# Kernel optimization log

Hardware: AMD Instinct MI355X
Metric: run time of the kernel (lower is better)

The kernel has to match this reference:

```python
import jax, jax.numpy as jnp
import numpy as np

B, S, D, H, DEPTH, VOCAB = 4096, 64, 512, 8, 4, 2
HD = D // H
EPS = 1e-5


def setup_inputs() -> dict:
    key = jax.random.key(0)
    ks = jax.random.split(key, 12)
    sc = 0.02
    return {
        "a_seq": jax.random.randint(ks[0], (B, S), 0, VOCAB, dtype=jnp.int32),
        "b_seq": jax.random.randint(ks[1], (B, S), 0, VOCAB, dtype=jnp.int32),
        "bit_emb": jax.random.normal(ks[2], (VOCAB, D), jnp.float32),
        "start_state": jax.random.normal(ks[3], (D,), jnp.float32),
        "ln1_g": jnp.ones((DEPTH, D), jnp.float32),
        "ln1_b": jnp.zeros((DEPTH, D), jnp.float32),
        # weights stored [in, out] (transpose of torch nn.Linear layout)
        "qkv_w": jax.random.normal(ks[4], (DEPTH, D, 3 * D), jnp.float32) * sc,
        "qkv_b": jnp.zeros((DEPTH, 3 * D), jnp.float32),
        "out_w": jax.random.normal(ks[5], (DEPTH, D, D), jnp.float32) * sc,
        "out_b": jnp.zeros((DEPTH, D), jnp.float32),
        "ln2_g": jnp.ones((DEPTH, D), jnp.float32),
        "ln2_b": jnp.zeros((DEPTH, D), jnp.float32),
        "ff1_w": jax.random.normal(ks[6], (DEPTH, D, 4 * D), jnp.float32) * sc,
        "ff1_b": jnp.zeros((DEPTH, 4 * D), jnp.float32),
        "ff2_w": jax.random.normal(ks[7], (DEPTH, 4 * D, D), jnp.float32) * sc,
        "ff2_b": jnp.zeros((DEPTH, D), jnp.float32),
        "head_w": jax.random.normal(ks[8], (D, 2), jnp.float32) * sc,
        "head_b": jnp.zeros((2,), jnp.float32),
    }


def _ln(x, g, b):
    m = x.mean(-1, keepdims=True)
    c = x - m
    v = (c * c).mean(-1, keepdims=True)
    return c * jax.lax.rsqrt(v + EPS) * g + b


def reference(a_seq, b_seq, bit_emb, start_state, ln1_g, ln1_b, qkv_w, qkv_b,
              out_w, out_b, ln2_g, ln2_b, ff1_w, ff1_b, ff2_w, ff2_b,
              head_w, head_b):
    # [B,S,D] combined bit embeddings, then time-major for scan
    emb = bit_emb[a_seq] + bit_emb[b_seq]
    xs = jnp.swapaxes(emb, 0, 1)  # [S,B,D]
    h0 = jnp.broadcast_to(start_state, (a_seq.shape[0], D))

    def step(h, xt):
        x = xt + h  # current_input = emb_a + emb_b + h_t, [B,D] (seq_len=1 squeezed)
        for l in range(DEPTH):  # pre-norm TransformerEncoderLayer, norm_first=True
            y = _ln(x, ln1_g[l], ln1_b[l])
            qkv = y @ qkv_w[l] + qkv_b[l]
            # self-attention over a single token: softmax of one score == 1,
            # so the attention output is exactly V (grads to Q,K are zero, as in torch)
            v = qkv[:, 2 * D:]
            x = x + v @ out_w[l] + out_b[l]
            y = _ln(x, ln2_g[l], ln2_b[l])
            x = x + jax.nn.relu(y @ ff1_w[l] + ff1_b[l]) @ ff2_w[l] + ff2_b[l]
        return x, x @ head_w + head_b

    _, logits = jax.lax.scan(step, h0, xs)  # [S,B,2]
    return jnp.swapaxes(logits, 0, 1)  # [B,S,2]
```

## Files before the change

### kernel.cpp

```cpp
#include <hip/hip_runtime.h>
#include <hip/hip_bf16.h>
#include <stdint.h>
#include <stddef.h>

#define B_ 4096
#define S_ 64
#define D_ 512
#define DEPTH_ 4


typedef __attribute__((ext_vector_type(8))) __bf16 bf16x8;
typedef __attribute__((ext_vector_type(4))) float f32x4;
typedef __hip_bfloat16 bf16_t;

constexpr int SPLITZ = 4;

__device__ __forceinline__ void async_copy16(const void* g, void* lds) {
  __builtin_amdgcn_global_load_lds(
      (const __attribute__((address_space(1))) void*)g,
      (__attribute__((address_space(3))) void*)lds, 16, 0, 0);
}

__device__ __forceinline__ float bf2f(bf16_t h) { return __bfloat162float(h); }

__device__ __forceinline__ void fold_p(float v[8], const bf16_t* pz)
{
  alignas(16) bf16_t t[8];
  *(uint4*)t = *(const uint4*)pz;
#pragma unroll
  for (int i = 0; i < 8; ++i) v[i] += bf2f(t[i]);
}

__device__ __forceinline__ void ln_vals(const float v[8],
                                        const float* __restrict__ gamma,
                                        const float* __restrict__ beta,
                                        int lane, bf16_t o8[8])
{
  float s = 0.f, ss = 0.f;
#pragma unroll
  for (int i = 0; i < 8; ++i) { s += v[i]; ss += v[i] * v[i]; }
#pragma unroll
  for (int o = 32; o; o >>= 1) { s += __shfl_xor(s, o); ss += __shfl_xor(ss, o); }
  const float m   = s * (1.f / D_);
  const float inv = rsqrtf(ss * (1.f / D_) - m * m + 1e-5f);
  const int c0 = lane * 8;
  float g[8], b[8];
  *(float4*)&g[0] = *(const float4*)&gamma[c0];
  *(float4*)&g[4] = *(const float4*)&gamma[c0 + 4];
  *(float4*)&b[0] = *(const float4*)&beta[c0];
  *(float4*)&b[4] = *(const float4*)&beta[c0 + 4];
#pragma unroll
  for (int i = 0; i < 8; ++i)
    o8[i] = __float2bfloat16((v[i] - m) * inv * g[i] + b[i]);
}

__device__ __forceinline__ void ln_store(const float v[8],
                                         const float* __restrict__ gamma,
                                         const float* __restrict__ beta,
                                         bf16_t* yrow, int lane)
{
  alignas(16) bf16_t o8[8];
  ln_vals(v, gamma, beta, lane, o8);
  *(uint4*)&yrow[lane * 8] = *(const uint4*)o8;
}

__device__ __forceinline__ void ln_store_swz(const float v[8],
                                             const float* __restrict__ gamma,
                                             const float* __restrict__ beta,
                                             bf16_t* srow, int row, int lane)
{
  alignas(16) bf16_t o8[8];
  ln_vals(v, gamma, beta, lane, o8);
  const int c0s = (lane * 8) ^ ((row & 7) << 3);
  *(uint4*)&srow[c0s] = *(const uint4*)o8;
}

template<int TM, int TN, int EPI, int SPLITK>
__launch_bounds__(256)
__global__ void gemm_bf16(const bf16_t* __restrict__ A,
                          const bf16_t* __restrict__ Bt,
                          const float* __restrict__ bias,
                          bf16_t* __restrict__ O,
                          int M, int N, int K)
{
  constexpr int BK  = 64;
  constexpr int WM  = TM / 2, WN = TN / 2;
  constexpr int NMI = WM / 16, NNI = WN / 16;
  constexpr int CA  = TM / 8, CB = TN / 8;
  static_assert(TM * TN <= (TM + TN) * BK, "C tile must fit in staging LDS");

  __shared__ __align__(16) bf16_t smem[(TM + TN) * BK];
  bf16_t* sA = smem;
  bf16_t* sB = smem + TM * BK;

  const int tid  = threadIdx.x;
  const int lane = tid & 63;
  const int wave = tid >> 6;
  const int wm   = wave & 1;
  const int wn   = wave >> 1;
  const int m0   = blockIdx.x * TM;
  const int n0   = blockIdx.y * TN;
  const int KS   = K / SPLITK;
  const int kbeg = blockIdx.z * KS;

  const int lr = lane >> 3;
  const int lc = (lane & 7) * 8;

  f32x4 acc[NMI][NNI];
#pragma unroll
  for (int mi = 0; mi < NMI; ++mi)
#pragma unroll
    for (int ni = 0; ni < NNI; ++ni)
      acc[mi][ni] = (f32x4){0.f, 0.f, 0.f, 0.f};

  for (int k0 = kbeg; k0 < kbeg + KS; k0 += BK) {
#pragma unroll
    for (int c = wave; c < CA; c += 4) {
      const bf16_t* g = A + (size_t)(m0 + c * 8 + lr) * K + (k0 + lc);
      async_copy16(g, (char*)sA + c * 1024);
    }
#pragma unroll
    for (int c = wave; c < CB; c += 4) {
      const bf16_t* g = Bt + (size_t)(n0 + c * 8 + lr) * K + (k0 + lc);
      async_copy16(g, (char*)sB + c * 1024);
    }
    __syncthreads();

#pragma unroll
    for (int kk = 0; kk < BK; kk += 32) {
      bf16x8 af[NMI], bfv[NNI];
#pragma unroll
      for (int mi = 0; mi < NMI; ++mi)
        af[mi] = *(const bf16x8*)&sA[(wm * WM + mi * 16 + (lane & 15)) * BK + kk + (lane >> 4) * 8];
#pragma unroll
      for (int ni = 0; ni < NNI; ++ni)
        bfv[ni] = *(const bf16x8*)&sB[(wn * WN + ni * 16 + (lane & 15)) * BK + kk + (lane >> 4) * 8];
#pragma unroll
      for (int mi = 0; mi < NMI; ++mi)
#pragma unroll
        for (int ni = 0; ni < NNI; ++ni)
          acc[mi][ni] = __builtin_amdgcn_mfma_f32_16x16x32_bf16(af[mi], bfv[ni], acc[mi][ni], 0, 0, 0);
    }
    __syncthreads();
  }

  bf16_t* sC = smem;
#pragma unroll
  for (int mi = 0; mi < NMI; ++mi) {
#pragma unroll
    for (int ni = 0; ni < NNI; ++ni) {
      const int col  = wn * WN + ni * 16 + (lane & 15);
      const int row0 = wm * WM + mi * 16 + ((lane >> 4) << 2);
      const float bv = (SPLITK == 1 || blockIdx.z == 0) ? bias[n0 + col] : 0.f;
#pragma unroll
      for (int r = 0; r < 4; ++r) {
        float v = acc[mi][ni][r] + bv;
        if constexpr (EPI == 1) v = v > 0.f ? v : 0.f;
        sC[(row0 + r) * TN + col] = __float2bfloat16(v);
      }
    }
  }
  __syncthreads();
  bf16_t* Ob = O + (EPI == 2 ? (size_t)blockIdx.z * M * N : (size_t)0);
#pragma unroll
  for (int p = 0; p < (TM * TN) / 2048; ++p) {
    const int chunk = p * 256 + tid;
    const int rr = chunk / (TN / 8);
    const int cc = (chunk % (TN / 8)) * 8;
    *(uint4*)&Ob[(size_t)(m0 + rr) * N + n0 + cc] = *(const uint4*)&sC[rr * TN + cc];
  }
}

__global__ void ln_sum1_kernel(float* __restrict__ X,
                               const bf16_t* __restrict__ P,
                               const float* __restrict__ gamma,
                               const float* __restrict__ beta,
                               bf16_t* __restrict__ Y)
{
  const int row  = blockIdx.x * 4 + (threadIdx.x >> 6);
  const int lane = threadIdx.x & 63;
  const int c0 = lane * 8;
  float* xr = X + (size_t)row * D_;
  float v[8];
  *(float4*)&v[0] = *(const float4*)&xr[c0];
  *(float4*)&v[4] = *(const float4*)&xr[c0 + 4];
  fold_p(v, P + (size_t)row * D_ + c0);
  *(float4*)&xr[c0]     = *(const float4*)&v[0];
  *(float4*)&xr[c0 + 4] = *(const float4*)&v[4];
  ln_store(v, gamma, beta, Y + (size_t)row * D_, lane);
}

__device__ __forceinline__ void small_gemm_loop(const bf16_t* __restrict__ sY,
                                                const bf16_t* __restrict__ Bt,
                                                int n0, int wave, int lane,
                                                f32x4 acc[2][2])
{
  const bf16_t* b0 = Bt + (size_t)(n0 + wave * 32 + (lane & 15)) * D_ + (lane >> 4) * 8;
  const bf16_t* b1 = b0 + (size_t)16 * D_;
  const int r0 = (lane & 15);
  const int r1 = 16 + (lane & 15);
  const int x0 = (r0 & 7) << 3;
  const int ka = (lane >> 4) * 8;
#pragma unroll
  for (int k0 = 0; k0 < D_; k0 += 32) {
    bf16x8 af0, af1, bv0, bv1;
    bv0 = *(const bf16x8*)&b0[k0];
    bv1 = *(const bf16x8*)&b1[k0];
    af0 = *(const bf16x8*)&sY[r0 * D_ + ((k0 + ka) ^ x0)];
    af1 = *(const bf16x8*)&sY[r1 * D_ + ((k0 + ka) ^ x0)];
    acc[0][0] = __builtin_amdgcn_mfma_f32_16x16x32_bf16(af0, bv0, acc[0][0], 0, 0, 0);
    acc[0][1] = __builtin_amdgcn_mfma_f32_16x16x32_bf16(af0, bv1, acc[0][1], 0, 0, 0);
    acc[1][0] = __builtin_amdgcn_mfma_f32_16x16x32_bf16(af1, bv0, acc[1][0], 0, 0, 0);
    acc[1][1] = __builtin_amdgcn_mfma_f32_16x16x32_bf16(af1, bv1, acc[1][1], 0, 0, 0);
  }
}

__device__ __forceinline__ void small_gemm_epi(bf16_t* sC, bf16_t* __restrict__ O,
                                               const float* __restrict__ bias,
                                               const f32x4 acc[2][2],
                                               int m0, int n0, int wave, int lane,
                                               int tid)
{
  constexpr int TM = 32, TN = 128;
#pragma unroll
  for (int mi = 0; mi < 2; ++mi) {
#pragma unroll
    for (int ni = 0; ni < 2; ++ni) {
      const int col  = wave * 32 + ni * 16 + (lane & 15);
      const int row0 = mi * 16 + ((lane >> 4) << 2);
      const float bv = bias[n0 + col];
#pragma unroll
      for (int r = 0; r < 4; ++r)
        sC[(row0 + r) * TN + col] = __float2bfloat16(acc[mi][ni][r] + bv);
    }
  }
  __syncthreads();
#pragma unroll
  for (int p = 0; p < (TM * TN) / 2048; ++p) {
    const int chunk = p * 256 + tid;
    const int rr = chunk / (TN / 8);
    const int cc = (chunk % (TN / 8)) * 8;
    *(uint4*)&O[(size_t)(m0 + rr) * D_ + n0 + cc] = *(const uint4*)&sC[rr * TN + cc];
  }
}

__launch_bounds__(256)
__global__ void lnfold_gemm(const float* __restrict__ Xin,
                            const bf16_t* __restrict__ P,
                            float* __restrict__ Xout,
                            const float* __restrict__ gamma,
                            const float* __restrict__ beta,
                            const bf16_t* __restrict__ Bt,
                            const float* __restrict__ bias,
                            bf16_t* __restrict__ O)
{
  constexpr int TM = 32;
  __shared__ __align__(16) bf16_t sY[TM * D_];

  const int tid  = threadIdx.x;
  const int lane = tid & 63;
  const int wave = tid >> 6;
  const int m0   = blockIdx.x * TM;
  const int n0   = blockIdx.y * 128;
  const int c0   = lane * 8;

#pragma unroll
  for (int i = 0; i < 8; ++i) {
    const int row  = wave * 8 + i;
    const int grow = m0 + row;
    const float* xr = Xin + (size_t)grow * D_ + c0;
    float v[8];
    *(float4*)&v[0] = *(const float4*)&xr[0];
    *(float4*)&v[4] = *(const float4*)&xr[4];
#pragma unroll
    for (int z = 0; z < SPLITZ; ++z)
      fold_p(v, P + (size_t)z * B_ * D_ + (size_t)grow * D_ + c0);
    if (blockIdx.y == 0) {
      float* xo = Xout + (size_t)grow * D_ + c0;
      *(float4*)&xo[0] = *(const float4*)&v[0];
      *(float4*)&xo[4] = *(const float4*)&v[4];
    }
    ln_store_swz(v, gamma, beta, &sY[row * D_], row, lane);
  }
  __syncthreads();

  f32x4 acc[2][2];
#pragma unroll
  for (int mi = 0; mi < 2; ++mi)
#pragma unroll
    for (int ni = 0; ni < 2; ++ni)
      acc[mi][ni] = (f32x4){0.f, 0.f, 0.f, 0.f};

  small_gemm_loop(sY, Bt, n0, wave, lane, acc);

  __syncthreads();
  small_gemm_epi(sY, O, bias, acc, m0, n0, wave, lane, tid);
}

__launch_bounds__(256)
__global__ void addln_gemm(const int* __restrict__ a_seq,
                           const int* __restrict__ b_seq,
                           const float* __restrict__ bit_emb,
                           const float* __restrict__ hsrc, int hstride,
                           const bf16_t* __restrict__ P,
                           float* __restrict__ Xout,
                           const float* __restrict__ gamma,
                           const float* __restrict__ beta,
                           const bf16_t* __restrict__ Bt,
                           const float* __restrict__ bias,
                           bf16_t* __restrict__ O,
                           int t,
                           const float* __restrict__ hw,
                           const float* __restrict__ hb,
                           float* __restrict__ out)
{
  constexpr int TM = 32;
  __shared__ __align__(16) bf16_t sY[TM * D_];

  const int tid  = threadIdx.x;
  const int lane = tid & 63;
  const int wave = tid >> 6;
  const int m0   = blockIdx.x * TM;
  const int n0   = blockIdx.y * 128;
  const int c0   = lane * 8;

  const bool do_head = (out != nullptr) && (blockIdx.y == 0);
  float w[16];
  if (do_head) {
#pragma unroll
    for (int i = 0; i < 4; ++i)
      *(float4*)&w[i * 4] = *(const float4*)&hw[lane * 16 + i * 4];
  }

#pragma unroll
  for (int i = 0; i < 8; ++i) {
    const int row  = wave * 8 + i;
    const int grow = m0 + row;
    const int ai = a_seq[grow * S_ + t];
    const int bi = b_seq[grow * S_ + t];
    const float* pr = hsrc + (size_t)grow * hstride + c0;
    float p[8];
    *(float4*)&p[0] = *(const float4*)&pr[0];
    *(float4*)&p[4] = *(const float4*)&pr[4];
    if (P != nullptr) {
#pragma unroll
      for (int z = 0; z < SPLITZ; ++z)
        fold_p(p, P + (size_t)z * B_ * D_ + (size_t)grow * D_ + c0);
    }
    if (do_head) {
      float s0 = 0.f, s1 = 0.f;
#pragma unroll
      for (int j = 0; j < 8; ++j) { s0 += p[j] * w[2 * j]; s1 += p[j] * w[2 * j + 1]; }
#pragma unroll
      for (int o = 32; o; o >>= 1) { s0 += __shfl_xor(s0, o); s1 += __shfl_xor(s1, o); }
      if (lane == 0) {
        float* po = out + (size_t)grow * (S_ * 2) + (t - 1) * 2;
        po[0] = s0 + hb[0];
        po[1] = s1 + hb[1];
      }
    }
    float ea[8], eb[8], v[8];
    *(float4*)&ea[0] = *(const float4*)&bit_emb[ai * D_ + c0];
    *(float4*)&ea[4] = *(const float4*)&bit_emb[ai * D_ + c0 + 4];
    *(float4*)&eb[0] = *(const float4*)&bit_emb[bi * D_ + c0];
    *(float4*)&eb[4] = *(const float4*)&bit_emb[bi * D_ + c0 + 4];
#pragma unroll
    for (int j = 0; j < 8; ++j) v[j] = ea[j] + eb[j] + p[j];
    if (blockIdx.y == 0) {
      float* xo = Xout + (size_t)grow * D_ + c0;
      *(float4*)&xo[0] = *(const float4*)&v[0];
      *(float4*)&xo[4] = *(const float4*)&v[4];
    }
    ln_store_swz(v, gamma, beta, &sY[row * D_], row, lane);
  }
  __syncthreads();

  f32x4 acc[2][2];
#pragma unroll
  for (int mi = 0; mi < 2; ++mi)
#pragma unroll
    for (int ni = 0; ni < 2; ++ni)
      acc[mi][ni] = (f32x4){0.f, 0.f, 0.f, 0.f};

  small_gemm_loop(sY, Bt, n0, wave, lane, acc);

  __syncthreads();
  small_gemm_epi(sY, O, bias, acc, m0, n0, wave, lane, tid);
}

__global__ void head_kernel(const float* __restrict__ X,
                            const bf16_t* __restrict__ P,
                            const float* __restrict__ hw,
                            const float* __restrict__ hb,
                            float* __restrict__ out, int t)
{
  const int row  = blockIdx.x * 4 + (threadIdx.x >> 6);
  const int lane = threadIdx.x & 63;
  const float* xr = X + (size_t)row * D_;
  const int c0 = lane * 8;
  float v[8];
  *(float4*)&v[0] = *(const float4*)&xr[c0];
  *(float4*)&v[4] = *(const float4*)&xr[c0 + 4];
#pragma unroll
  for (int z = 0; z < SPLITZ; ++z)
    fold_p(v, P + (size_t)z * B_ * D_ + (size_t)row * D_ + c0);
  float w[16];
#pragma unroll
  for (int i = 0; i < 4; ++i)
    *(float4*)&w[i * 4] = *(const float4*)&hw[lane * 16 + i * 4];
  float s0 = 0.f, s1 = 0.f;
#pragma unroll
  for (int i = 0; i < 8; ++i) { s0 += v[i] * w[2 * i]; s1 += v[i] * w[2 * i + 1]; }
#pragma unroll
  for (int o = 32; o; o >>= 1) { s0 += __shfl_xor(s0, o); s1 += __shfl_xor(s1, o); }
  if (lane == 0) {
    float* po = out + (size_t)row * (S_ * 2) + t * 2;
    po[0] = s0 + hb[0];
    po[1] = s1 + hb[1];
  }
}

__global__ void prep_wc(const float* __restrict__ qkv_w,
                        const float* __restrict__ out_w,
                        float* __restrict__ wc)
{
  const int n = blockIdx.x * 256 + threadIdx.x;
  const int k = blockIdx.y;
  const int l = blockIdx.z;
  const float* qrow = qkv_w + ((size_t)l * D_ + k) * (3 * D_) + 2 * D_;
  const float* ow   = out_w + (size_t)l * D_ * D_;
  float acc = 0.f;
  for (int j = 0; j < D_; ++j) acc += qrow[j] * ow[(size_t)j * D_ + n];
  wc[((size_t)l * D_ + k) * D_ + n] = acc;
}

__global__ void prep_bc(const float* __restrict__ qkv_b,
                        const float* __restrict__ out_w,
                        const float* __restrict__ out_b,
                        float* __restrict__ bc)
{
  const int l = blockIdx.x;
  const int n = threadIdx.x;
  const float* qb = qkv_b + (size_t)l * (3 * D_) + 2 * D_;
  const float* ow = out_w + (size_t)l * D_ * D_;
  float acc = out_b[(size_t)l * D_ + n];
  for (int j = 0; j < D_; ++j) acc += qb[j] * ow[(size_t)j * D_ + n];
  bc[(size_t)l * D_ + n] = acc;
}

__global__ void transpose_conv(const float* __restrict__ src,
                               bf16_t* __restrict__ dst, int R, int C)
{
  __shared__ float tile[32][33];
  const int l = blockIdx.z;
  const float* s = src + (size_t)l * R * C;
  bf16_t* d = dst + (size_t)l * R * C;
  const int c0 = blockIdx.x * 32, r0 = blockIdx.y * 32;
  const int tx = threadIdx.x, ty = threadIdx.y;
  tile[ty][tx] = s[(size_t)(r0 + ty) * C + (c0 + tx)];
  __syncthreads();
  d[(size_t)(c0 + ty) * R + (r0 + tx)] = __float2bfloat16(tile[tx][ty]);
}

extern "C" void kernel_launch(void* const* d_in, const int* in_sizes, int n_in,
                              void* d_out, int out_size, void* d_ws, size_t ws_size,
                              hipStream_t stream)
{
  const int*   a_seq     = (const int*)  d_in[0];
  const int*   b_seq     = (const int*)  d_in[1];
  const float* bit_emb   = (const float*)d_in[2];
  const float* start     = (const float*)d_in[3];
  const float* ln1_g     = (const float*)d_in[4];
  const float* ln1_b     = (const float*)d_in[5];
  const float* qkv_w     = (const float*)d_in[6];
  const float* qkv_b     = (const float*)d_in[7];
  const float* out_w     = (const float*)d_in[8];
  const float* out_b     = (const float*)d_in[9];
  const float* ln2_g     = (const float*)d_in[10];
  const float* ln2_b     = (const float*)d_in[11];
  const float* ff1_w     = (const float*)d_in[12];
  const float* ff1_b     = (const float*)d_in[13];
  const float* ff2_w     = (const float*)d_in[14];
  const float* ff2_b     = (const float*)d_in[15];
  const float* head_w    = (const float*)d_in[16];
  const float* head_b    = (const float*)d_in[17];
  float* out = (float*)d_out;

  char* ws = (char*)d_ws;
  float*  XA    = (float*) ws; ws += (size_t)B_ * D_ * 4;
  float*  XB    = (float*) ws; ws += (size_t)B_ * D_ * 4;
  bf16_t* Y     = (bf16_t*)ws; ws += (size_t)B_ * D_ * 2;
  bf16_t* U     = (bf16_t*)ws; ws += (size_t)B_ * 4 * D_ * 2;
  bf16_t* WCT   = (bf16_t*)ws; ws += (size_t)DEPTH_ * D_ * D_ * 2;
  bf16_t* FF1T  = (bf16_t*)ws; ws += (size_t)DEPTH_ * D_ * 4 * D_ * 2;
  bf16_t* FF2T  = (bf16_t*)ws; ws += (size_t)DEPTH_ * 4 * D_ * D_ * 2;
  float*  BC    = (float*) ws; ws += (size_t)DEPTH_ * D_ * 4;
  float*  WCTMP = (float*) ws; ws += (size_t)DEPTH_ * D_ * D_ * 4;
  bf16_t* PSPL  = (bf16_t*)ws; ws += (size_t)SPLITZ * B_ * D_ * 2;
  bf16_t* P1    = (bf16_t*)ws; ws += (size_t)B_ * D_ * 2;

  prep_wc<<<dim3(2, 512, 4), 256, 0, stream>>>(qkv_w, out_w, WCTMP);
  prep_bc<<<4, 512, 0, stream>>>(qkv_b, out_w, out_b, BC);
  transpose_conv<<<dim3(16, 16, 4),  dim3(32, 32), 0, stream>>>(WCTMP, WCT, 512, 512);
  transpose_conv<<<dim3(64, 16, 4),  dim3(32, 32), 0, stream>>>(ff1_w, FF1T, 512, 2048);
  transpose_conv<<<dim3(16, 64, 4),  dim3(32, 32), 0, stream>>>(ff2_w, FF2T, 2048, 512);

  for (int t = 0; t < S_; ++t) {
    if (t == 0)
      addln_gemm<<<dim3(B_ / 32, 4), 256, 0, stream>>>(
          a_seq, b_seq, bit_emb, start, 0, nullptr, XA,
          ln1_g, ln1_b, WCT, BC, P1, t, head_w, head_b, nullptr);
    else
      addln_gemm<<<dim3(B_ / 32, 4), 256, 0, stream>>>(
          a_seq, b_seq, bit_emb, XB, D_, PSPL, XA,
          ln1_g, ln1_b, WCT, BC, P1, t, head_w, head_b, out);
    float* cur = XA;
    float* alt = XB;
    for (int l = 0; l < DEPTH_; ++l) {
      if (l > 0) {
        lnfold_gemm<<<dim3(B_ / 32, 4), 256, 0, stream>>>(
            cur, PSPL, alt,
            ln1_g + (size_t)l * D_, ln1_b + (size_t)l * D_,
            WCT + (size_t)l * D_ * D_, BC + (size_t)l * D_, P1);
        float* tmp = cur; cur = alt; alt = tmp;
      }
      ln_sum1_kernel<<<B_ / 4, 256, 0, stream>>>(cur, P1,
                                                 ln2_g + (size_t)l * D_,
                                                 ln2_b + (size_t)l * D_, Y);
      gemm_bf16<128, 128, 1, 1><<<dim3(32, 16), 256, 0, stream>>>(
          Y, FF1T + (size_t)l * D_ * 4 * D_, ff1_b + (size_t)l * 4 * D_, U,
          B_, 4 * D_, D_);
      gemm_bf16<128, 128, 2, SPLITZ><<<dim3(32, 4, SPLITZ), 256, 0, stream>>>(
          U, FF2T + (size_t)l * 4 * D_ * D_, ff2_b + (size_t)l * D_, PSPL,
          B_, D_, 4 * D_);
    }
  }
  head_kernel<<<B_ / 4, 256, 0, stream>>>(XB, PSPL, head_w, head_b, out, S_ - 1);
}
```

Baseline: 14.75 ms.

## Fuse attention-projection GEMM with residual add and LN2 into one layer kernel

Merges the LN1+small GEMM kernel and the separate residual-fold+LN2 kernel into one fused_layer kernel. Each block now owns 16 full rows and computes all 512 output columns, so the residual add and second layernorm can run in the epilogue through an fp32 shared-memory tile. This removes one launch per layer, the P1 bf16 intermediate round trip, and the XA/XB ping-pong buffers. In exchange it uses fewer, larger blocks (256 instead of 512), each with more accumulators and more shared memory, and the weight tile is reread by more blocks.

```diff
diff --git a/kernel.cpp b/kernel.cpp
--- a/kernel.cpp
+++ b/kernel.cpp
@@ -171,221 +171,140 @@
   }
 }
 
-__global__ void ln_sum1_kernel(float* __restrict__ X,
-                               const bf16_t* __restrict__ P,
-                               const float* __restrict__ gamma,
-                               const float* __restrict__ beta,
-                               bf16_t* __restrict__ Y)
-{
-  const int row  = blockIdx.x * 4 + (threadIdx.x >> 6);
-  const int lane = threadIdx.x & 63;
-  const int c0 = lane * 8;
-  float* xr = X + (size_t)row * D_;
-  float v[8];
-  *(float4*)&v[0] = *(const float4*)&xr[c0];
-  *(float4*)&v[4] = *(const float4*)&xr[c0 + 4];
-  fold_p(v, P + (size_t)row * D_ + c0);
-  *(float4*)&xr[c0]     = *(const float4*)&v[0];
-  *(float4*)&xr[c0 + 4] = *(const float4*)&v[4];
-  ln_store(v, gamma, beta, Y + (size_t)row * D_, lane);
-}
-
-__device__ __forceinline__ void small_gemm_loop(const bf16_t* __restrict__ sY,
-                                                const bf16_t* __restrict__ Bt,
-                                                int n0, int wave, int lane,
-                                                f32x4 acc[2][2])
-{
-  const bf16_t* b0 = Bt + (size_t)(n0 + wave * 32 + (lane & 15)) * D_ + (lane >> 4) * 8;
-  const bf16_t* b1 = b0 + (size_t)16 * D_;
-  const int r0 = (lane & 15);
-  const int r1 = 16 + (lane & 15);
-  const int x0 = (r0 & 7) << 3;
-  const int ka = (lane >> 4) * 8;
-#pragma unroll
-  for (int k0 = 0; k0 < D_; k0 += 32) {
-    bf16x8 af0, af1, bv0, bv1;
-    bv0 = *(const bf16x8*)&b0[k0];
-    bv1 = *(const bf16x8*)&b1[k0];
-    af0 = *(const bf16x8*)&sY[r0 * D_ + ((k0 + ka) ^ x0)];
-    af1 = *(const bf16x8*)&sY[r1 * D_ + ((k0 + ka) ^ x0)];
-    acc[0][0] = __builtin_amdgcn_mfma_f32_16x16x32_bf16(af0, bv0, acc[0][0], 0, 0, 0);
-    acc[0][1] = __builtin_amdgcn_mfma_f32_16x16x32_bf16(af0, bv1, acc[0][1], 0, 0, 0);
-    acc[1][0] = __builtin_amdgcn_mfma_f32_16x16x32_bf16(af1, bv0, acc[1][0], 0, 0, 0);
-    acc[1][1] = __builtin_amdgcn_mfma_f32_16x16x32_bf16(af1, bv1, acc[1][1], 0, 0, 0);
-  }
-}
-
-__device__ __forceinline__ void small_gemm_epi(bf16_t* sC, bf16_t* __restrict__ O,
-                                               const float* __restrict__ bias,
-                                               const f32x4 acc[2][2],
-                                               int m0, int n0, int wave, int lane,
-                                               int tid)
-{
-  constexpr int TM = 32, TN = 128;
-#pragma unroll
-  for (int mi = 0; mi < 2; ++mi) {
-#pragma unroll
-    for (int ni = 0; ni < 2; ++ni) {
-      const int col  = wave * 32 + ni * 16 + (lane & 15);
-      const int row0 = mi * 16 + ((lane >> 4) << 2);
-      const float bv = bias[n0 + col];
-#pragma unroll
-      for (int r = 0; r < 4; ++r)
-        sC[(row0 + r) * TN + col] = __float2bfloat16(acc[mi][ni][r] + bv);
-    }
-  }
-  __syncthreads();
-#pragma unroll
-  for (int p = 0; p < (TM * TN) / 2048; ++p) {
-    const int chunk = p * 256 + tid;
-    const int rr = chunk / (TN / 8);
-    const int cc = (chunk % (TN / 8)) * 8;
-    *(uint4*)&O[(size_t)(m0 + rr) * D_ + n0 + cc] = *(const uint4*)&sC[rr * TN + cc];
-  }
-}
-
+template<bool L0>
 __launch_bounds__(256)
-__global__ void lnfold_gemm(const float* __restrict__ Xin,
+__global__ void fused_layer(float* __restrict__ X,
                             const bf16_t* __restrict__ P,
-                            float* __restrict__ Xout,
-                            const float* __restrict__ gamma,
-                            const float* __restrict__ beta,
+                            const float* __restrict__ g1,
+                            const float* __restrict__ b1,
                             const bf16_t* __restrict__ Bt,
                             const float* __restrict__ bias,
-                            bf16_t* __restrict__ O)
-{
-  constexpr int TM = 32;
+                            const float* __restrict__ g2v,
+                            const float* __restrict__ b2v,
+                            bf16_t* __restrict__ Y,
+                            const int* __restrict__ a_seq,
+                            const int* __restrict__ b_seq,
+                            const float* __restrict__ bit_emb,
+                            const float* __restrict__ hsrc, int hstride,
+                            int t,
+                            const float* __restrict__ hw,
+                            const float* __restrict__ hb,
+                            float* __restrict__ out)
+{
+  constexpr int TM  = 16;
+  constexpr int SPS = D_ + 4;
   __shared__ __align__(16) bf16_t sY[TM * D_];
+  __shared__ __align__(16) float  sP[TM * SPS];
 
   const int tid  = threadIdx.x;
   const int lane = tid & 63;
   const int wave = tid >> 6;
   const int m0   = blockIdx.x * TM;
-  const int n0   = blockIdx.y * 128;
   const int c0   = lane * 8;
 
-#pragma unroll
-  for (int i = 0; i < 8; ++i) {
-    const int row  = wave * 8 + i;
-    const int grow = m0 + row;
-    const float* xr = Xin + (size_t)grow * D_ + c0;
-    float v[8];
-    *(float4*)&v[0] = *(const float4*)&xr[0];
-    *(float4*)&v[4] = *(const float4*)&xr[4];
-#pragma unroll
-    for (int z = 0; z < SPLITZ; ++z)
-      fold_p(v, P + (size_t)z * B_ * D_ + (size_t)grow * D_ + c0);
-    if (blockIdx.y == 0) {
-      float* xo = Xout + (size_t)grow * D_ + c0;
-      *(float4*)&xo[0] = *(const float4*)&v[0];
-      *(float4*)&xo[4] = *(const float4*)&v[4];
-    }
-    ln_store_swz(v, gamma, beta, &sY[row * D_], row, lane);
-  }
-  __syncthreads();
-
-  f32x4 acc[2][2];
-#pragma unroll
-  for (int mi = 0; mi < 2; ++mi)
-#pragma unroll
-    for (int ni = 0; ni < 2; ++ni)
-      acc[mi][ni] = (f32x4){0.f, 0.f, 0.f, 0.f};
-
-  small_gemm_loop(sY, Bt, n0, wave, lane, acc);
-
-  __syncthreads();
-  small_gemm_epi(sY, O, bias, acc, m0, n0, wave, lane, tid);
-}
-
-__launch_bounds__(256)
-__global__ void addln_gemm(const int* __restrict__ a_seq,
-                           const int* __restrict__ b_seq,
-                           const float* __restrict__ bit_emb,
-                           const float* __restrict__ hsrc, int hstride,
-                           const bf16_t* __restrict__ P,
-                           float* __restrict__ Xout,
-                           const float* __restrict__ gamma,
-                           const float* __restrict__ beta,
-                           const bf16_t* __restrict__ Bt,
-                           const float* __restrict__ bias,
-                           bf16_t* __restrict__ O,
-                           int t,
-                           const float* __restrict__ hw,
-                           const float* __restrict__ hb,
-                           float* __restrict__ out)
-{
-  constexpr int TM = 32;
-  __shared__ __align__(16) bf16_t sY[TM * D_];
-
-  const int tid  = threadIdx.x;
-  const int lane = tid & 63;
-  const int wave = tid >> 6;
-  const int m0   = blockIdx.x * TM;
-  const int n0   = blockIdx.y * 128;
-  const int c0   = lane * 8;
-
-  const bool do_head = (out != nullptr) && (blockIdx.y == 0);
   float w[16];
+  const bool do_head = L0 && (out != nullptr);
   if (do_head) {
 #pragma unroll
     for (int i = 0; i < 4; ++i)
       *(float4*)&w[i * 4] = *(const float4*)&hw[lane * 16 + i * 4];
   }
 
-#pragma unroll
-  for (int i = 0; i < 8; ++i) {
-    const int row  = wave * 8 + i;
+  float vx[4][8];
+#pragma unroll
+  for (int i = 0; i < 4; ++i) {
+    const int row  = wave * 4 + i;
     const int grow = m0 + row;
-    const int ai = a_seq[grow * S_ + t];
-    const int bi = b_seq[grow * S_ + t];
-    const float* pr = hsrc + (size_t)grow * hstride + c0;
-    float p[8];
-    *(float4*)&p[0] = *(const float4*)&pr[0];
-    *(float4*)&p[4] = *(const float4*)&pr[4];
-    if (P != nullptr) {
+    float v[8];
+    if constexpr (L0) {
+      const float* pr = hsrc + (size_t)grow * hstride + c0;
+      float p[8];
+      *(float4*)&p[0] = *(const float4*)&pr[0];
+      *(float4*)&p[4] = *(const float4*)&pr[4];
+      if (P != nullptr) {
+#pragma unroll
+        for (int z = 0; z < SPLITZ; ++z)
+          fold_p(p, P + (size_t)z * B_ * D_ + (size_t)grow * D_ + c0);
+      }
+      if (do_head) {
+        float s0 = 0.f, s1 = 0.f;
+#pragma unroll
+        for (int j = 0; j < 8; ++j) { s0 += p[j] * w[2 * j]; s1 += p[j] * w[2 * j + 1]; }
+#pragma unroll
+        for (int o = 32; o; o >>= 1) { s0 += __shfl_xor(s0, o); s1 += __shfl_xor(s1, o); }
+        if (lane == 0) {
+          float* po = out + (size_t)grow * (S_ * 2) + (t - 1) * 2;
+          po[0] = s0 + hb[0];
+          po[1] = s1 + hb[1];
+        }
+      }
+      const int ai = a_seq[grow * S_ + t];
+      const int bi = b_seq[grow * S_ + t];
+      float ea[8], eb[8];
+      *(float4*)&ea[0] = *(const float4*)&bit_emb[ai * D_ + c0];
+      *(float4*)&ea[4] = *(const float4*)&bit_emb[ai * D_ + c0 + 4];
+      *(float4*)&eb[0] = *(const float4*)&bit_emb[bi * D_ + c0];
+      *(float4*)&eb[4] = *(const float4*)&bit_emb[bi * D_ + c0 + 4];
+#pragma unroll
+      for (int j = 0; j < 8; ++j) v[j] = ea[j] + eb[j] + p[j];
+    } else {
+      const float* xr = X + (size_t)grow * D_ + c0;
+      *(float4*)&v[0] = *(const float4*)&xr[0];
+      *(float4*)&v[4] = *(const float4*)&xr[4];
 #pragma unroll
       for (int z = 0; z < SPLITZ; ++z)
-        fold_p(p, P + (size_t)z * B_ * D_ + (size_t)grow * D_ + c0);
-    }
-    if (do_head) {
-      float s0 = 0.f, s1 = 0.f;
-#pragma unroll
-      for (int j = 0; j < 8; ++j) { s0 += p[j] * w[2 * j]; s1 += p[j] * w[2 * j + 1]; }
-#pragma unroll
-      for (int o = 32; o; o >>= 1) { s0 += __shfl_xor(s0, o); s1 += __shfl_xor(s1, o); }
-      if (lane == 0) {
-        float* po = out + (size_t)grow * (S_ * 2) + (t - 1) * 2;
-        po[0] = s0 + hb[0];
-        po[1] = s1 + hb[1];
-      }
-    }
-    float ea[8], eb[8], v[8];
-    *(float4*)&ea[0] = *(const float4*)&bit_emb[ai * D_ + c0];
-    *(float4*)&ea[4] = *(const float4*)&bit_emb[ai * D_ + c0 + 4];
-    *(float4*)&eb[0] = *(const float4*)&bit_emb[bi * D_ + c0];
-    *(float4*)&eb[4] = *(const float4*)&bit_emb[bi * D_ + c0 + 4];
-#pragma unroll
-    for (int j = 0; j < 8; ++j) v[j] = ea[j] + eb[j] + p[j];
-    if (blockIdx.y == 0) {
-      float* xo = Xout + (size_t)grow * D_ + c0;
-      *(float4*)&xo[0] = *(const float4*)&v[0];
-      *(float4*)&xo[4] = *(const float4*)&v[4];
-    }
-    ln_store_swz(v, gamma, beta, &sY[row * D_], row, lane);
+        fold_p(v, P + (size_t)z * B_ * D_ + (size_t)grow * D_ + c0);
+    }
+#pragma unroll
+    for (int j = 0; j < 8; ++j) vx[i][j] = v[j];
+    ln_store_swz(v, g1, b1, &sY[row * D_], row, lane);
   }
   __syncthreads();
 
-  f32x4 acc[2][2];
-#pragma unroll
-  for (int mi = 0; mi < 2; ++mi)
-#pragma unroll
-    for (int ni = 0; ni < 2; ++ni)
-      acc[mi][ni] = (f32x4){0.f, 0.f, 0.f, 0.f};
-
-  small_gemm_loop(sY, Bt, n0, wave, lane, acc);
-
+  f32x4 acc[8];
+#pragma unroll
+  for (int ni = 0; ni < 8; ++ni) acc[ni] = (f32x4){0.f, 0.f, 0.f, 0.f};
+
+  const bf16_t* bb = Bt + (size_t)(wave * 128 + (lane & 15)) * D_ + (lane >> 4) * 8;
+  const int r0 = lane & 15;
+  const int x0 = (r0 & 7) << 3;
+  const int ka = (lane >> 4) * 8;
+#pragma unroll
+  for (int k0 = 0; k0 < D_; k0 += 32) {
+    const bf16x8 af = *(const bf16x8*)&sY[r0 * D_ + ((k0 + ka) ^ x0)];
+#pragma unroll
+    for (int ni = 0; ni < 8; ++ni) {
+      const bf16x8 bv = *(const bf16x8*)&bb[(size_t)ni * 16 * D_ + k0];
+      acc[ni] = __builtin_amdgcn_mfma_f32_16x16x32_bf16(af, bv, acc[ni], 0, 0, 0);
+    }
+  }
+
+  const int prow0 = (lane >> 4) << 2;
+#pragma unroll
+  for (int ni = 0; ni < 8; ++ni) {
+    const int col = wave * 128 + ni * 16 + (lane & 15);
+    const float bv = bias[col];
+#pragma unroll
+    for (int r = 0; r < 4; ++r)
+      sP[(prow0 + r) * SPS + col] = acc[ni][r] + bv;
+  }
   __syncthreads();
-  small_gemm_epi(sY, O, bias, acc, m0, n0, wave, lane, tid);
+
+#pragma unroll
+  for (int i = 0; i < 4; ++i) {
+    const int row  = wave * 4 + i;
+    const int grow = m0 + row;
+    const float* pr = &sP[row * SPS + c0];
+    float v[8];
+    *(float4*)&v[0] = *(const float4*)&pr[0];
+    *(float4*)&v[4] = *(const float4*)&pr[4];
+#pragma unroll
+    for (int j = 0; j < 8; ++j) v[j] += vx[i][j];
+    float* xo = X + (size_t)grow * D_ + c0;
+    *(float4*)&xo[0] = *(const float4*)&v[0];
+    *(float4*)&xo[4] = *(const float4*)&v[4];
+    ln_store(v, g2v, b2v, &Y[(size_t)grow * D_], lane);
+  }
 }
 
 __global__ void head_kernel(const float* __restrict__ X,
@@ -487,8 +406,7 @@
   float* out = (float*)d_out;
 
   char* ws = (char*)d_ws;
-  float*  XA    = (float*) ws; ws += (size_t)B_ * D_ * 4;
-  float*  XB    = (float*) ws; ws += (size_t)B_ * D_ * 4;
+  float*  X     = (float*) ws; ws += (size_t)B_ * D_ * 4;
   bf16_t* Y     = (bf16_t*)ws; ws += (size_t)B_ * D_ * 2;
   bf16_t* U     = (bf16_t*)ws; ws += (size_t)B_ * 4 * D_ * 2;
   bf16_t* WCT   = (bf16_t*)ws; ws += (size_t)DEPTH_ * D_ * D_ * 2;
@@ -497,7 +415,6 @@
   float*  BC    = (float*) ws; ws += (size_t)DEPTH_ * D_ * 4;
   float*  WCTMP = (float*) ws; ws += (size_t)DEPTH_ * D_ * D_ * 4;
   bf16_t* PSPL  = (bf16_t*)ws; ws += (size_t)SPLITZ * B_ * D_ * 2;
-  bf16_t* P1    = (bf16_t*)ws; ws += (size_t)B_ * D_ * 2;
 
   prep_wc<<<dim3(2, 512, 4), 256, 0, stream>>>(qkv_w, out_w, WCTMP);
   prep_bc<<<4, 512, 0, stream>>>(qkv_b, out_w, out_b, BC);
@@ -506,27 +423,24 @@
   transpose_conv<<<dim3(16, 64, 4),  dim3(32, 32), 0, stream>>>(ff2_w, FF2T, 2048, 512);
 
   for (int t = 0; t < S_; ++t) {
-    if (t == 0)
-      addln_gemm<<<dim3(B_ / 32, 4), 256, 0, stream>>>(
-          a_seq, b_seq, bit_emb, start, 0, nullptr, XA,
-          ln1_g, ln1_b, WCT, BC, P1, t, head_w, head_b, nullptr);
-    else
-      addln_gemm<<<dim3(B_ / 32, 4), 256, 0, stream>>>(
-          a_seq, b_seq, bit_emb, XB, D_, PSPL, XA,
-          ln1_g, ln1_b, WCT, BC, P1, t, head_w, head_b, out);
-    float* cur = XA;
-    float* alt = XB;
     for (int l = 0; l < DEPTH_; ++l) {
-      if (l > 0) {
-        lnfold_gemm<<<dim3(B_ / 32, 4), 256, 0, stream>>>(
-            cur, PSPL, alt,
+      if (l == 0) {
+        if (t == 0)
+          fused_layer<true><<<B_ / 16, 256, 0, stream>>>(
+              X, nullptr, ln1_g, ln1_b, WCT, BC, ln2_g, ln2_b, Y,
+              a_seq, b_seq, bit_emb, start, 0, t, head_w, head_b, nullptr);
+        else
+          fused_layer<true><<<B_ / 16, 256, 0, stream>>>(
+              X, PSPL, ln1_g, ln1_b, WCT, BC, ln2_g, ln2_b, Y,
+              a_seq, b_seq, bit_emb, X, D_, t, head_w, head_b, out);
+      } else {
+        fused_layer<false><<<B_ / 16, 256, 0, stream>>>(
+            X, PSPL,
             ln1_g + (size_t)l * D_, ln1_b + (size_t)l * D_,
-            WCT + (size_t)l * D_ * D_, BC + (size_t)l * D_, P1);
-        float* tmp = cur; cur = alt; alt = tmp;
+            WCT + (size_t)l * D_ * D_, BC + (size_t)l * D_,
+            ln2_g + (size_t)l * D_, ln2_b + (size_t)l * D_, Y,
+            nullptr, nullptr, nullptr, nullptr, 0, 0, nullptr, nullptr, nullptr);
       }
-      ln_sum1_kernel<<<B_ / 4, 256, 0, stream>>>(cur, P1,
-                                                 ln2_g + (size_t)l * D_,
-                                                 ln2_b + (size_t)l * D_, Y);
       gemm_bf16<128, 128, 1, 1><<<dim3(32, 16), 256, 0, stream>>>(
           Y, FF1T + (size_t)l * D_ * 4 * D_, ff1_b + (size_t)l * 4 * D_, U,
           B_, 4 * D_, D_);
@@ -535,5 +449,5 @@
           B_, D_, 4 * D_);
     }
   }
-  head_kernel<<<B_ / 4, 256, 0, stream>>>(XB, PSPL, head_w, head_b, out, S_ - 1);
-}
+  head_kernel<<<B_ / 4, 256, 0, stream>>>(X, PSPL, head_w, head_b, out, S_ - 1);
+}
```

Result: slower. 18.74 ms (+27.0%).

## Replace LDS-staged FFN GEMM with direct global-to-register MFMA operand loads

Applied to the files above, without the earlier changes.

The FFN GEMMs no longer stage A and B tiles through LDS with async copies and barriers. Each wave now loads its MFMA operand fragments straight from global memory into registers, and LDS is kept only for the output tile. This is meant to remove LDS round trips and __syncthreads overhead. The cost is that operands are no longer shared across waves, so each A/B row is fetched twice from global/L2, and the per-lane 16-byte loads are strided by K.

```diff
diff --git a/kernel.cpp b/kernel.cpp
--- a/kernel.cpp
+++ b/kernel.cpp
@@ -75,23 +75,16 @@
   *(uint4*)&srow[c0s] = *(const uint4*)o8;
 }
 
-template<int TM, int TN, int EPI, int SPLITK>
+template<int EPI, int SPLITK>
 __launch_bounds__(256)
-__global__ void gemm_bf16(const bf16_t* __restrict__ A,
-                          const bf16_t* __restrict__ Bt,
-                          const float* __restrict__ bias,
-                          bf16_t* __restrict__ O,
-                          int M, int N, int K)
-{
-  constexpr int BK  = 64;
-  constexpr int WM  = TM / 2, WN = TN / 2;
-  constexpr int NMI = WM / 16, NNI = WN / 16;
-  constexpr int CA  = TM / 8, CB = TN / 8;
-  static_assert(TM * TN <= (TM + TN) * BK, "C tile must fit in staging LDS");
-
-  __shared__ __align__(16) bf16_t smem[(TM + TN) * BK];
-  bf16_t* sA = smem;
-  bf16_t* sB = smem + TM * BK;
+__global__ void gemm_direct(const bf16_t* __restrict__ A,
+                            const bf16_t* __restrict__ Bt,
+                            const float* __restrict__ bias,
+                            bf16_t* __restrict__ O,
+                            int M, int N, int K)
+{
+  constexpr int TM = 128, TN = 128;
+  __shared__ __align__(16) bf16_t sC[TM * TN];
 
   const int tid  = threadIdx.x;
   const int lane = tid & 63;
@@ -103,54 +96,39 @@
   const int KS   = K / SPLITK;
   const int kbeg = blockIdx.z * KS;
 
-  const int lr = lane >> 3;
-  const int lc = (lane & 7) * 8;
-
-  f32x4 acc[NMI][NNI];
-#pragma unroll
-  for (int mi = 0; mi < NMI; ++mi)
-#pragma unroll
-    for (int ni = 0; ni < NNI; ++ni)
+  const int kl = (lane >> 4) * 8;
+  const bf16_t* Ab = A  + (size_t)(m0 + wm * 64 + (lane & 15)) * K + kl;
+  const bf16_t* Bb = Bt + (size_t)(n0 + wn * 64 + (lane & 15)) * K + kl;
+
+  f32x4 acc[4][4];
+#pragma unroll
+  for (int mi = 0; mi < 4; ++mi)
+#pragma unroll
+    for (int ni = 0; ni < 4; ++ni)
       acc[mi][ni] = (f32x4){0.f, 0.f, 0.f, 0.f};
 
-  for (int k0 = kbeg; k0 < kbeg + KS; k0 += BK) {
-#pragma unroll
-    for (int c = wave; c < CA; c += 4) {
-      const bf16_t* g = A + (size_t)(m0 + c * 8 + lr) * K + (k0 + lc);
-      async_copy16(g, (char*)sA + c * 1024);
-    }
-#pragma unroll
-    for (int c = wave; c < CB; c += 4) {
-      const bf16_t* g = Bt + (size_t)(n0 + c * 8 + lr) * K + (k0 + lc);
-      async_copy16(g, (char*)sB + c * 1024);
-    }
-    __syncthreads();
-
-#pragma unroll
-    for (int kk = 0; kk < BK; kk += 32) {
-      bf16x8 af[NMI], bfv[NNI];
-#pragma unroll
-      for (int mi = 0; mi < NMI; ++mi)
-        af[mi] = *(const bf16x8*)&sA[(wm * WM + mi * 16 + (lane & 15)) * BK + kk + (lane >> 4) * 8];
-#pragma unroll
-      for (int ni = 0; ni < NNI; ++ni)
-        bfv[ni] = *(const bf16x8*)&sB[(wn * WN + ni * 16 + (lane & 15)) * BK + kk + (lane >> 4) * 8];
-#pragma unroll
-      for (int mi = 0; mi < NMI; ++mi)
-#pragma unroll
-        for (int ni = 0; ni < NNI; ++ni)
-          acc[mi][ni] = __builtin_amdgcn_mfma_f32_16x16x32_bf16(af[mi], bfv[ni], acc[mi][ni], 0, 0, 0);
-    }
-    __syncthreads();
-  }
-
-  bf16_t* sC = smem;
-#pragma unroll
-  for (int mi = 0; mi < NMI; ++mi) {
-#pragma unroll
-    for (int ni = 0; ni < NNI; ++ni) {
-      const int col  = wn * WN + ni * 16 + (lane & 15);
-      const int row0 = wm * WM + mi * 16 + ((lane >> 4) << 2);
+#pragma unroll 4
+  for (int k0 = kbeg; k0 < kbeg + KS; k0 += 32) {
+    bf16x8 af[4], bfv[4];
+#pragma unroll
+    for (int mi = 0; mi < 4; ++mi)
+      af[mi] = *(const bf16x8*)&Ab[(size_t)(mi * 16) * K + k0];
+#pragma unroll
+    for (int ni = 0; ni < 4; ++ni)
+      bfv[ni] = *(const bf16x8*)&Bb[(size_t)(ni * 16) * K + k0];
+#pragma unroll
+    for (int mi = 0; mi < 4; ++mi)
+#pragma unroll
+      for (int ni = 0; ni < 4; ++ni)
+        acc[mi][ni] = __builtin_amdgcn_mfma_f32_16x16x32_bf16(af[mi], bfv[ni], acc[mi][ni], 0, 0, 0);
+  }
+
+#pragma unroll
+  for (int mi = 0; mi < 4; ++mi) {
+#pragma unroll
+    for (int ni = 0; ni < 4; ++ni) {
+      const int col  = wn * 64 + ni * 16 + (lane & 15);
+      const int row0 = wm * 64 + mi * 16 + ((lane >> 4) << 2);
       const float bv = (SPLITK == 1 || blockIdx.z == 0) ? bias[n0 + col] : 0.f;
 #pragma unroll
       for (int r = 0; r < 4; ++r) {
@@ -527,10 +505,10 @@
       ln_sum1_kernel<<<B_ / 4, 256, 0, stream>>>(cur, P1,
                                                  ln2_g + (size_t)l * D_,
                                                  ln2_b + (size_t)l * D_, Y);
-      gemm_bf16<128, 128, 1, 1><<<dim3(32, 16), 256, 0, stream>>>(
+      gemm_direct<1, 1><<<dim3(32, 16), 256, 0, stream>>>(
           Y, FF1T + (size_t)l * D_ * 4 * D_, ff1_b + (size_t)l * 4 * D_, U,
           B_, 4 * D_, D_);
-      gemm_bf16<128, 128, 2, SPLITZ><<<dim3(32, 4, SPLITZ), 256, 0, stream>>>(
+      gemm_direct<2, SPLITZ><<<dim3(32, 4, SPLITZ), 256, 0, stream>>>(
           U, FF2T + (size_t)l * 4 * D_ * D_, ff2_b + (size_t)l * D_, PSPL,
           B_, D_, 4 * D_);
     }
```

After: 23.24 ms. +57.5%, slower.

## Double-buffer GEMM LDS staging to overlap global loads with MFMA compute

Applied to the files above, without the earlier changes.

Switches the bf16 GEMM main loop to two LDS staging buffers. It issues async global-to-LDS loads for the next K tile before computing the current one, using explicit vmcnt waits and raw barriers. The aim is to hide global memory latency behind the matrix-core work instead of stalling on every tile. It doubles LDS use per block, which may lower occupancy, and it relies on a hardcoded vmcnt value that assumes exactly 8 loads per wave per tile.

```diff
diff --git a/kernel.cpp b/kernel.cpp
--- a/kernel.cpp
+++ b/kernel.cpp
@@ -87,11 +87,11 @@
   constexpr int WM  = TM / 2, WN = TN / 2;
   constexpr int NMI = WM / 16, NNI = WN / 16;
   constexpr int CA  = TM / 8, CB = TN / 8;
-  static_assert(TM * TN <= (TM + TN) * BK, "C tile must fit in staging LDS");
-
-  __shared__ __align__(16) bf16_t smem[(TM + TN) * BK];
-  bf16_t* sA = smem;
-  bf16_t* sB = smem + TM * BK;
+  constexpr int BUF = (TM + TN) * BK;
+  static_assert((CA + CB) / 4 == 8, "vmcnt(8) assumes 8 loads/wave/tile");
+  static_assert(TM * TN <= BUF, "C tile must fit in one staging buffer");
+
+  __shared__ __align__(16) bf16_t smem[2 * BUF];
 
   const int tid  = threadIdx.x;
   const int lane = tid & 63;
@@ -102,6 +102,7 @@
   const int n0   = blockIdx.y * TN;
   const int KS   = K / SPLITK;
   const int kbeg = blockIdx.z * KS;
+  const int NI   = KS / BK;
 
   const int lr = lane >> 3;
   const int lc = (lane & 7) * 8;
@@ -113,19 +114,34 @@
     for (int ni = 0; ni < NNI; ++ni)
       acc[mi][ni] = (f32x4){0.f, 0.f, 0.f, 0.f};
 
-  for (int k0 = kbeg; k0 < kbeg + KS; k0 += BK) {
-#pragma unroll
-    for (int c = wave; c < CA; c += 4) {
-      const bf16_t* g = A + (size_t)(m0 + c * 8 + lr) * K + (k0 + lc);
-      async_copy16(g, (char*)sA + c * 1024);
-    }
-#pragma unroll
-    for (int c = wave; c < CB; c += 4) {
-      const bf16_t* g = Bt + (size_t)(n0 + c * 8 + lr) * K + (k0 + lc);
-      async_copy16(g, (char*)sB + c * 1024);
-    }
-    __syncthreads();
-
+  auto STAGE = [&](int k0, int b) {
+    bf16_t* sA = smem + b * BUF;
+    bf16_t* sB = sA + TM * BK;
+#pragma unroll
+    for (int c = wave; c < CA; c += 4)
+      async_copy16(A + (size_t)(m0 + c * 8 + lr) * K + (k0 + lc),
+                   (char*)sA + c * 1024);
+#pragma unroll
+    for (int c = wave; c < CB; c += 4)
+      async_copy16(Bt + (size_t)(n0 + c * 8 + lr) * K + (k0 + lc),
+                   (char*)sB + c * 1024);
+  };
+
+  STAGE(kbeg, 0);
+
+  for (int i = 0; i < NI; ++i) {
+    const int cur = i & 1;
+    if (i + 1 < NI) {
+      STAGE(kbeg + (i + 1) * BK, cur ^ 1);
+      asm volatile("s_waitcnt vmcnt(8)" ::: "memory");
+    } else {
+      asm volatile("s_waitcnt vmcnt(0)" ::: "memory");
+    }
+    __builtin_amdgcn_s_barrier();
+    __builtin_amdgcn_sched_barrier(0);
+
+    const bf16_t* sA = smem + cur * BUF;
+    const bf16_t* sB = sA + TM * BK;
 #pragma unroll
     for (int kk = 0; kk < BK; kk += 32) {
       bf16x8 af[NMI], bfv[NNI];
@@ -141,7 +157,8 @@
         for (int ni = 0; ni < NNI; ++ni)
           acc[mi][ni] = __builtin_amdgcn_mfma_f32_16x16x32_bf16(af[mi], bfv[ni], acc[mi][ni], 0, 0, 0);
     }
-    __syncthreads();
+    __builtin_amdgcn_sched_barrier(0);
+    __builtin_amdgcn_s_barrier();
   }
 
   bf16_t* sC = smem;
```

New measurement: 14.16 ms. 4.0% less time.
